# Optimization experiments

Hardware: AMD Instinct MI355X
Metric: run time of the kernel (lower is better)

The kernel has to match this reference:

```python
import jax, jax.numpy as jnp
import numpy as np

B, S, E, H, D = 4, 2048, 1152, 12, 96
ROPE_BASE = 10000.0


def setup_inputs() -> dict:
    key = jax.random.key(0)
    ks = jax.random.split(key, 5)
    init = lambda k, shape: jax.random.normal(k, shape, dtype=jnp.float32) * 0.02
    return {
        "logits": jax.random.normal(ks[0], (B, S, E), dtype=jnp.float32),
        "Wq": init(ks[1], (E, H * D)), "bq": jnp.zeros((H * D,), jnp.float32),
        "Wk": init(ks[2], (E, H * D)), "bk": jnp.zeros((H * D,), jnp.float32),
        "Wv": init(ks[3], (E, H * D)), "bv": jnp.zeros((H * D,), jnp.float32),
        "Wo": init(ks[4], (H * D, E)), "bo": jnp.zeros((E,), jnp.float32),
        "batch_size": B,
        "seq_len": S,
    }


def _rope(x, cos, sin):
    # x: [b, s, h, d]; cos/sin: [s, d//2]; interleaved-pair rotation
    b, s, h, d = x.shape
    xr = x.reshape(b, s, h, d // 2, 2)
    c = cos[None, :, None, :]
    sn = sin[None, :, None, :]
    o0 = xr[..., 0] * c - xr[..., 1] * sn
    o1 = xr[..., 1] * c + xr[..., 0] * sn
    return jnp.stack([o0, o1], axis=-1).reshape(b, s, h, d)


def reference(logits, Wq, bq, Wk, bk, Wv, bv, Wo, bo, batch_size, seq_len):
    b, s = batch_size, seq_len
    q = (logits @ Wq + bq).reshape(b, s, H, D)
    k = (logits @ Wk + bk).reshape(b, s, H, D)
    v = (logits @ Wv + bv).reshape(b, s, H, D)

    # RoPE cache (cos/sin) for positions 0..s-1
    theta = 1.0 / (ROPE_BASE ** (jnp.arange(0, D, 2, dtype=jnp.float32) / D))  # [D/2]
    angles = jnp.arange(s, dtype=jnp.float32)[:, None] * theta[None, :]        # [s, D/2]
    cos, sin = jnp.cos(angles), jnp.sin(angles)

    q = _rope(q, cos, sin)
    k = _rope(k, cos, sin)

    # causal SDPA, scale = 1/sqrt(head_dim)
    scale = 1.0 / jnp.sqrt(jnp.asarray(D, jnp.float32))
    scores = jnp.einsum("bqhd,bkhd->bhqk", q, k) * scale  # [b, h, s, s]
    causal = jnp.tril(jnp.ones((s, s), dtype=bool))
    scores = jnp.where(causal[None, None], scores, -jnp.inf)
    attn = jax.nn.softmax(scores, axis=-1)
    ctx = jnp.einsum("bhqk,bkhd->bqhd", attn, v).reshape(b, s, H * D)
    return ctx @ Wo + bo
```

## Files before the change

### kernel.cpp

```cpp
#include <hip/hip_runtime.h>

typedef __bf16 bf16;
typedef bf16 bf16x4 __attribute__((ext_vector_type(4)));
typedef bf16 bf16x8 __attribute__((ext_vector_type(8)));
typedef float f32x4 __attribute__((ext_vector_type(4)));

#define B_  4
#define S_  2048
#define E_  1152
#define H_  12
#define D_  96
#define HD_ 1152
#define M_  (B_*S_)
#define BH_ (B_*H_)

__device__ __forceinline__ void gl2lds16(const void* g, void* l) {
    __builtin_amdgcn_global_load_lds((const __attribute__((address_space(1))) void*)g,
                                     (__attribute__((address_space(3))) void*)l, 16, 0, 0);
}

__global__ __launch_bounds__(256) void cast_bf16_k(const float* __restrict__ in,
                                                   bf16* __restrict__ out) {
    size_t i = ((size_t)blockIdx.x * 256 + threadIdx.x) * 4;
    float4 v = *(const float4*)(in + i);
    bf16x4 o = { (bf16)v.x, (bf16)v.y, (bf16)v.z, (bf16)v.w };
    *(bf16x4*)(out + i) = o;
}

__global__ __launch_bounds__(256) void rope_tab_k(float2* __restrict__ tab) {
    int idx = blockIdx.x * 256 + threadIdx.x;
    int s = idx / 48, i = idx % 48;
    float theta = powf(10000.0f, -(float)(2 * i) / 96.0f);
    float ang = (float)s * theta;
    tab[idx] = make_float2(cosf(ang), sinf(ang));
}

__global__ __launch_bounds__(256) void transpose_w_all_k(const float* __restrict__ W0,
        const float* __restrict__ W1, const float* __restrict__ W2, const float* __restrict__ W3,
        bf16* __restrict__ T0, bf16* __restrict__ T1, bf16* __restrict__ T2, bf16* __restrict__ T3) {
    const float* W; bf16* WT;
    switch (blockIdx.z) {
        case 0: W = W0; WT = T0; break;
        case 1: W = W1; WT = T1; break;
        case 2: W = W2; WT = T2; break;
        default: W = W3; WT = T3; break;
    }
    __shared__ float t[32][33];
    int bx = blockIdx.x * 32;
    int by = blockIdx.y * 32;
    int tx = threadIdx.x, ty = threadIdx.y;
    #pragma unroll
    for (int i = ty; i < 32; i += 8)
        t[i][tx] = W[(size_t)(by + i) * E_ + bx + tx];
    __syncthreads();
    #pragma unroll
    for (int i = ty; i < 32; i += 8)
        WT[(size_t)(bx + i) * E_ + by + tx] = (bf16)t[tx][i];
}

__global__ __launch_bounds__(256) void transpose_v_k(const bf16* __restrict__ v,
                                                     bf16* __restrict__ VT) {
    __shared__ bf16 t[32][33];
    int bh = blockIdx.z;
    int b = bh / H_, h = bh % H_;
    int s0 = blockIdx.x * 32, d0 = blockIdx.y * 32;
    int tx = threadIdx.x, ty = threadIdx.y;
    #pragma unroll
    for (int i = ty; i < 32; i += 8)
        t[i][tx] = v[(size_t)(b * S_ + s0 + i) * HD_ + h * D_ + d0 + tx];
    __syncthreads();
    #pragma unroll
    for (int i = ty; i < 32; i += 8)
        VT[(size_t)(bh * D_ + d0 + i) * S_ + s0 + tx] = t[tx][i];
}

__device__ __forceinline__ void gemm128_body(const bf16* __restrict__ X,
                                             const bf16* __restrict__ WT,
                                             const float* __restrict__ bias,
                                             bf16* __restrict__ Cb,
                                             float* __restrict__ Cf,
                                             const float2* __restrict__ ctab,
                                             int K, int rope) {
    __shared__ bf16 As[128 * 32];
    __shared__ bf16 Bs[128 * 32];
    const int N = 1152;
    int t = threadIdx.x;
    int lane = t & 63, wave = t >> 6;
    int quad = lane >> 4, l16 = lane & 15;
    int wm = wave >> 1, wn = wave & 1;
    int m0 = blockIdx.x * 128, n0 = blockIdx.y * 128;

    const bf16* ga = X  + (size_t)(m0 + (t >> 2)) * K + (t & 3) * 8;
    const bf16* gb = WT + (size_t)(n0 + (t >> 2)) * K + (t & 3) * 8;
    bf16* la = As + t * 8;
    bf16* lb = Bs + t * 8;
    size_t rowskip = (size_t)64 * K;

    f32x4 acc[4][4];
    #pragma unroll
    for (int u = 0; u < 4; ++u)
        #pragma unroll
        for (int v = 0; v < 4; ++v) acc[u][v] = (f32x4){0.f, 0.f, 0.f, 0.f};

    for (int k0 = 0; k0 < K; k0 += 32) {
        __syncthreads();
        gl2lds16(ga + k0,           la);
        gl2lds16(ga + k0 + rowskip, la + 64 * 32);
        gl2lds16(gb + k0,           lb);
        gl2lds16(gb + k0 + rowskip, lb + 64 * 32);
        __syncthreads();
        bf16x8 af[4], bfr[4];
        #pragma unroll
        for (int u = 0; u < 4; ++u)
            af[u] = *(const bf16x8*)(As + (wm * 64 + u * 16 + l16) * 32 + quad * 8);
        #pragma unroll
        for (int v = 0; v < 4; ++v)
            bfr[v] = *(const bf16x8*)(Bs + (wn * 64 + v * 16 + l16) * 32 + quad * 8);
        #pragma unroll
        for (int u = 0; u < 4; ++u)
            #pragma unroll
            for (int v = 0; v < 4; ++v)
                acc[u][v] = __builtin_amdgcn_mfma_f32_16x16x32_bf16(af[u], bfr[v], acc[u][v], 0, 0, 0);
    }

    int mrow = m0 + wm * 64, ncol = n0 + wn * 64;
    if (Cf) {
        #pragma unroll
        for (int v = 0; v < 4; ++v) {
            int n = ncol + v * 16 + l16;
            float bv = bias[n];
            #pragma unroll
            for (int u = 0; u < 4; ++u)
                #pragma unroll
                for (int r = 0; r < 4; ++r)
                    Cf[(size_t)(mrow + u * 16 + quad * 4 + r) * N + n] = acc[u][v][r] + bv;
        }
    } else if (rope) {
        #pragma unroll
        for (int v = 0; v < 4; ++v) {
            int n = ncol + v * 16 + l16;
            float bv = bias[n];
            int i = (n % 96) >> 1;
            float sgn = (n & 1) ? 1.f : -1.f;
            #pragma unroll
            for (int u = 0; u < 4; ++u)
                #pragma unroll
                for (int r = 0; r < 4; ++r) {
                    int m = mrow + u * 16 + quad * 4 + r;
                    float x = acc[u][v][r] + bv;
                    float p = __shfl_xor(x, 1, 64);
                    float2 cs = ctab[(m & (S_ - 1)) * 48 + i];
                    Cb[(size_t)m * N + n] = (bf16)(x * cs.x + p * sgn * cs.y);
                }
        }
    } else {
        #pragma unroll
        for (int v = 0; v < 4; ++v) {
            int n = ncol + v * 16 + l16;
            float bv = bias[n];
            #pragma unroll
            for (int u = 0; u < 4; ++u)
                #pragma unroll
                for (int r = 0; r < 4; ++r)
                    Cb[(size_t)(mrow + u * 16 + quad * 4 + r) * N + n] = (bf16)(acc[u][v][r] + bv);
        }
    }
}

__global__ __launch_bounds__(256) void gemm_qkv_k(const bf16* __restrict__ X,
        const bf16* __restrict__ Wq, const bf16* __restrict__ Wk, const bf16* __restrict__ Wv,
        const float* __restrict__ bq, const float* __restrict__ bk, const float* __restrict__ bv,
        bf16* __restrict__ q, bf16* __restrict__ k, bf16* __restrict__ v,
        const float2* __restrict__ ctab) {
    const bf16* W; const float* bias; bf16* C; int rope;
    if (blockIdx.z == 0)      { W = Wq; bias = bq; C = q; rope = 1; }
    else if (blockIdx.z == 1) { W = Wk; bias = bk; C = k; rope = 1; }
    else                      { W = Wv; bias = bv; C = v; rope = 0; }
    gemm128_body(X, W, bias, C, nullptr, ctab, E_, rope);
}

__global__ __launch_bounds__(256) void gemm_out_k(const bf16* __restrict__ X,
        const bf16* __restrict__ WT, const float* __restrict__ bias, float* __restrict__ Cf) {
    gemm128_body(X, WT, bias, nullptr, Cf, nullptr, HD_, 0);
}

__global__ __launch_bounds__(256) void flash3_k(const bf16* __restrict__ Q,
                                                const bf16* __restrict__ Kg,
                                                const bf16* __restrict__ VT,
                                                bf16* __restrict__ ctx) {
    __shared__ bf16 Ks[64 * 104];
    __shared__ bf16 Vs[96 * 72];
    __shared__ bf16 Ps[4][16][72];
    int t = threadIdx.x, lane = t & 63, wave = t >> 6;
    int quad = lane >> 4, l16 = lane & 15;
    int bh = blockIdx.x % BH_;
    int ch = (S_ / 64 - 1) - blockIdx.x / BH_;
    int b = bh / H_, h = bh % H_;
    int q0 = ch * 64;
    int qw = q0 + wave * 16;
    int qabs = qw + l16;

    const char* KbaseB = (const char*)(Kg + (size_t)(b * S_) * HD_ + h * D_);
    const char* VbaseB = (const char*)(VT + (size_t)(bh * D_) * S_);

    int krow[4], koff[4], vrow[4], voff[4];
    #pragma unroll
    for (int i = 0; i < 4; ++i) {
        int c = i * 256 + t;
        krow[i] = c / 13; koff[i] = (c % 13) * 16;
        vrow[i] = c / 9;  int cc = c % 9; voff[i] = ((cc == 8) ? 7 : cc) * 16;
    }

    const bf16* qrow = Q + (size_t)(b * S_ + qw + l16) * HD_ + h * D_;
    bf16x8 qf[3];
    #pragma unroll
    for (int c = 0; c < 3; ++c)
        qf[c] = *(const bf16x8*)(qrow + c * 32 + quad * 8);

    f32x4 o[6];
    #pragma unroll
    for (int u = 0; u < 6; ++u) o[u] = (f32x4){0.f, 0.f, 0.f, 0.f};
    float lsum = 0.f;
    const float K2 = 0.10206207261596575f * 1.4426950408889634f;
    int nk = q0 + 64;

    for (int kb = 0; kb < nk; kb += 64) {
        __syncthreads();
        const char* kg = KbaseB + (size_t)kb * (HD_ * 2);
        #pragma unroll
        for (int i = 0; i < 3; ++i)
            gl2lds16(kg + (size_t)krow[i] * (HD_ * 2) + koff[i], (char*)Ks + i * 4096 + t * 16);
        if (t < 64)
            gl2lds16(kg + (size_t)krow[3] * (HD_ * 2) + koff[3], (char*)Ks + 12288 + t * 16);
        #pragma unroll
        for (int i = 0; i < 4; ++i)
            if (i < 3 || t < 96)
                gl2lds16(VbaseB + (size_t)vrow[i] * (S_ * 2) + (size_t)kb * 2 + voff[i],
                         (char*)Vs + i * 4096 + t * 16);
        __syncthreads();

        f32x4 st[4];
        #pragma unroll
        for (int u = 0; u < 4; ++u) st[u] = (f32x4){0.f, 0.f, 0.f, 0.f};
        #pragma unroll
        for (int c = 0; c < 3; ++c)
            #pragma unroll
            for (int u = 0; u < 4; ++u) {
                bf16x8 kf = *(const bf16x8*)(Ks + (u * 16 + l16) * 104 + c * 32 + quad * 8);
                st[u] = __builtin_amdgcn_mfma_f32_16x16x32_bf16(kf, qf[c], st[u], 0, 0, 0);
            }

        #pragma unroll
        for (int u = 0; u < 4; ++u) {
            bf16x4 pv;
            #pragma unroll
            for (int r = 0; r < 4; ++r) {
                int sidx = kb + u * 16 + quad * 4 + r;
                float e = __builtin_exp2f(st[u][r] * K2);
                e = (sidx <= qabs) ? e : 0.f;
                lsum += e;
                pv[r] = (bf16)e;
            }
            *(bf16x4*)(&Ps[wave][l16][u * 16 + quad * 4]) = pv;
        }
        asm volatile("s_waitcnt lgkmcnt(0)" ::: "memory");

        bf16x8 p0 = *(const bf16x8*)(&Ps[wave][l16][quad * 8]);
        bf16x8 p1 = *(const bf16x8*)(&Ps[wave][l16][32 + quad * 8]);
        #pragma unroll
        for (int u = 0; u < 6; ++u) {
            bf16x8 v0 = *(const bf16x8*)(Vs + (u * 16 + l16) * 72 + quad * 8);
            o[u] = __builtin_amdgcn_mfma_f32_16x16x32_bf16(v0, p0, o[u], 0, 0, 0);
            bf16x8 v1 = *(const bf16x8*)(Vs + (u * 16 + l16) * 72 + 32 + quad * 8);
            o[u] = __builtin_amdgcn_mfma_f32_16x16x32_bf16(v1, p1, o[u], 0, 0, 0);
        }
    }

    lsum += __shfl_xor(lsum, 16, 64);
    lsum += __shfl_xor(lsum, 32, 64);
    float inv = 1.0f / lsum;

    bf16* crow = ctx + (size_t)(b * S_ + qw + l16) * HD_ + h * D_;
    #pragma unroll
    for (int u = 0; u < 6; ++u) {
        bf16x4 ov;
        #pragma unroll
        for (int r = 0; r < 4; ++r) ov[r] = (bf16)(o[u][r] * inv);
        *(bf16x4*)(crow + u * 16 + quad * 4) = ov;
    }
}

extern "C" void kernel_launch(void* const* d_in, const int* in_sizes, int n_in,
                              void* d_out, int out_size, void* d_ws, size_t ws_size,
                              hipStream_t stream) {
    const float* logits = (const float*)d_in[0];
    const float* Wq = (const float*)d_in[1];
    const float* bq = (const float*)d_in[2];
    const float* Wk = (const float*)d_in[3];
    const float* bk = (const float*)d_in[4];
    const float* Wv = (const float*)d_in[5];
    const float* bv = (const float*)d_in[6];
    const float* Wo = (const float*)d_in[7];
    const float* bo = (const float*)d_in[8];
    float* out = (float*)d_out;

    char* ws = (char*)d_ws;
    size_t off = 0;
    auto alloc = [&](size_t bytes) { char* p = ws + off; off += (bytes + 255) & ~(size_t)255; return p; };
    bf16* Xbf = (bf16*)alloc((size_t)M_ * E_ * 2);
    bf16* WqT = (bf16*)alloc((size_t)E_ * HD_ * 2);
    bf16* WkT = (bf16*)alloc((size_t)E_ * HD_ * 2);
    bf16* WvT = (bf16*)alloc((size_t)E_ * HD_ * 2);
    bf16* WoT = (bf16*)alloc((size_t)HD_ * E_ * 2);
    bf16* qb  = (bf16*)alloc((size_t)M_ * HD_ * 2);
    bf16* kb  = (bf16*)alloc((size_t)M_ * HD_ * 2);
    bf16* vb  = (bf16*)alloc((size_t)M_ * HD_ * 2);
    bf16* VT  = (bf16*)alloc((size_t)M_ * HD_ * 2);
    float2* ctab = (float2*)alloc((size_t)S_ * 48 * 8);
    bf16* ctx = Xbf;

    hipLaunchKernelGGL(cast_bf16_k, dim3((M_ * (size_t)E_) / 1024), dim3(256), 0, stream, logits, Xbf);
    hipLaunchKernelGGL(rope_tab_k, dim3((S_ * 48) / 256), dim3(256), 0, stream, ctab);
    hipLaunchKernelGGL(transpose_w_all_k, dim3(36, 36, 4), dim3(32, 8), 0, stream,
                       Wq, Wk, Wv, Wo, WqT, WkT, WvT, WoT);
    hipLaunchKernelGGL(gemm_qkv_k, dim3(M_ / 128, 1152 / 128, 3), dim3(256), 0, stream,
                       Xbf, WqT, WkT, WvT, bq, bk, bv, qb, kb, vb, ctab);
    hipLaunchKernelGGL(transpose_v_k, dim3(S_ / 32, D_ / 32, BH_), dim3(32, 8), 0, stream, vb, VT);
    hipLaunchKernelGGL(flash3_k, dim3(BH_ * (S_ / 64)), dim3(256), 0, stream, qb, kb, VT, ctx);
    hipLaunchKernelGGL(gemm_out_k, dim3(M_ / 128, 1152 / 128), dim3(256), 0, stream, ctx, WoT, bo, out);
}
```

Before: 367.6 us.

## Double GEMM K-tile to 64 with XOR-swizzled LDS layout and flattened QKV grid

The shared GEMM body now stages 64-wide K tiles instead of 32, halving the number of barrier pairs per output tile. Loads are redistributed so each thread fetches 8 elements from an XOR-swizzled column, and fragment reads use the same swizzle to avoid LDS bank conflicts on the longer 128-byte rows. The QKV launch folds the z dimension into y (27 column tiles), so consecutive blocks share the same X rows. LDS use doubles to 32 KB per block, which may lower occupancy.

```diff
diff --git a/kernel.cpp b/kernel.cpp
--- a/kernel.cpp
+++ b/kernel.cpp
@@ -80,21 +80,22 @@
                                              bf16* __restrict__ Cb,
                                              float* __restrict__ Cf,
                                              const float2* __restrict__ ctab,
-                                             int K, int rope) {
-    __shared__ bf16 As[128 * 32];
-    __shared__ bf16 Bs[128 * 32];
+                                             int K, int rope, int m0, int n0) {
+    __shared__ bf16 As[128 * 64];
+    __shared__ bf16 Bs[128 * 64];
     const int N = 1152;
     int t = threadIdx.x;
     int lane = t & 63, wave = t >> 6;
     int quad = lane >> 4, l16 = lane & 15;
     int wm = wave >> 1, wn = wave & 1;
-    int m0 = blockIdx.x * 128, n0 = blockIdx.y * 128;
-
-    const bf16* ga = X  + (size_t)(m0 + (t >> 2)) * K + (t & 3) * 8;
-    const bf16* gb = WT + (size_t)(n0 + (t >> 2)) * K + (t & 3) * 8;
+
+    int srow = t >> 3;
+    int scol = ((t & 7) ^ (srow & 7)) * 8;
+    const bf16* ga = X  + (size_t)(m0 + srow) * K + scol;
+    const bf16* gb = WT + (size_t)(n0 + srow) * K + scol;
     bf16* la = As + t * 8;
     bf16* lb = Bs + t * 8;
-    size_t rowskip = (size_t)64 * K;
+    size_t skip = (size_t)32 * K;
 
     f32x4 acc[4][4];
     #pragma unroll
@@ -102,25 +103,30 @@
         #pragma unroll
         for (int v = 0; v < 4; ++v) acc[u][v] = (f32x4){0.f, 0.f, 0.f, 0.f};
 
-    for (int k0 = 0; k0 < K; k0 += 32) {
+    for (int k0 = 0; k0 < K; k0 += 64) {
         __syncthreads();
-        gl2lds16(ga + k0,           la);
-        gl2lds16(ga + k0 + rowskip, la + 64 * 32);
-        gl2lds16(gb + k0,           lb);
-        gl2lds16(gb + k0 + rowskip, lb + 64 * 32);
+        #pragma unroll
+        for (int i = 0; i < 4; ++i) {
+            gl2lds16(ga + k0 + i * skip, la + i * 2048);
+            gl2lds16(gb + k0 + i * skip, lb + i * 2048);
+        }
         __syncthreads();
-        bf16x8 af[4], bfr[4];
-        #pragma unroll
-        for (int u = 0; u < 4; ++u)
-            af[u] = *(const bf16x8*)(As + (wm * 64 + u * 16 + l16) * 32 + quad * 8);
-        #pragma unroll
-        for (int v = 0; v < 4; ++v)
-            bfr[v] = *(const bf16x8*)(Bs + (wn * 64 + v * 16 + l16) * 32 + quad * 8);
-        #pragma unroll
-        for (int u = 0; u < 4; ++u)
+        #pragma unroll
+        for (int kk = 0; kk < 2; ++kk) {
+            int xc = ((kk * 4 + quad) ^ (l16 & 7)) * 8;
+            bf16x8 af[4], bfr[4];
+            #pragma unroll
+            for (int u = 0; u < 4; ++u)
+                af[u] = *(const bf16x8*)(As + (wm * 64 + u * 16 + l16) * 64 + xc);
             #pragma unroll
             for (int v = 0; v < 4; ++v)
-                acc[u][v] = __builtin_amdgcn_mfma_f32_16x16x32_bf16(af[u], bfr[v], acc[u][v], 0, 0, 0);
+                bfr[v] = *(const bf16x8*)(Bs + (wn * 64 + v * 16 + l16) * 64 + xc);
+            #pragma unroll
+            for (int u = 0; u < 4; ++u)
+                #pragma unroll
+                for (int v = 0; v < 4; ++v)
+                    acc[u][v] = __builtin_amdgcn_mfma_f32_16x16x32_bf16(af[u], bfr[v], acc[u][v], 0, 0, 0);
+        }
     }
 
     int mrow = m0 + wm * 64, ncol = n0 + wn * 64;
@@ -172,16 +178,18 @@
         const float* __restrict__ bq, const float* __restrict__ bk, const float* __restrict__ bv,
         bf16* __restrict__ q, bf16* __restrict__ k, bf16* __restrict__ v,
         const float2* __restrict__ ctab) {
+    int zone = blockIdx.y / 9;
+    int n0 = (blockIdx.y % 9) * 128;
     const bf16* W; const float* bias; bf16* C; int rope;
-    if (blockIdx.z == 0)      { W = Wq; bias = bq; C = q; rope = 1; }
-    else if (blockIdx.z == 1) { W = Wk; bias = bk; C = k; rope = 1; }
-    else                      { W = Wv; bias = bv; C = v; rope = 0; }
-    gemm128_body(X, W, bias, C, nullptr, ctab, E_, rope);
+    if (zone == 0)      { W = Wq; bias = bq; C = q; rope = 1; }
+    else if (zone == 1) { W = Wk; bias = bk; C = k; rope = 1; }
+    else                { W = Wv; bias = bv; C = v; rope = 0; }
+    gemm128_body(X, W, bias, C, nullptr, ctab, E_, rope, blockIdx.x * 128, n0);
 }
 
 __global__ __launch_bounds__(256) void gemm_out_k(const bf16* __restrict__ X,
         const bf16* __restrict__ WT, const float* __restrict__ bias, float* __restrict__ Cf) {
-    gemm128_body(X, WT, bias, nullptr, Cf, nullptr, HD_, 0);
+    gemm128_body(X, WT, bias, nullptr, Cf, nullptr, HD_, 0, blockIdx.x * 128, blockIdx.y * 128);
 }
 
 __global__ __launch_bounds__(256) void flash3_k(const bf16* __restrict__ Q,
@@ -323,7 +331,7 @@
     hipLaunchKernelGGL(rope_tab_k, dim3((S_ * 48) / 256), dim3(256), 0, stream, ctab);
     hipLaunchKernelGGL(transpose_w_all_k, dim3(36, 36, 4), dim3(32, 8), 0, stream,
                        Wq, Wk, Wv, Wo, WqT, WkT, WvT, WoT);
-    hipLaunchKernelGGL(gemm_qkv_k, dim3(M_ / 128, 1152 / 128, 3), dim3(256), 0, stream,
+    hipLaunchKernelGGL(gemm_qkv_k, dim3(M_ / 128, 27), dim3(256), 0, stream,
                        Xbf, WqT, WkT, WvT, bq, bk, bv, qb, kb, vb, ctab);
     hipLaunchKernelGGL(transpose_v_k, dim3(S_ / 32, D_ / 32, BH_), dim3(32, 8), 0, stream, vb, VT);
     hipLaunchKernelGGL(flash3_k, dim3(BH_ * (S_ / 64)), dim3(256), 0, stream, qb, kb, VT, ctx);
```

After: 342.3 us. 1.07x faster.
